# Performance work log

Measured on AMD Instinct MI355X. Metric: run time of the kernel, lower is better.

## Reference

```python
import jax, jax.numpy as jnp
import numpy as np

N, E, DIN, DH, DE, DOUT, G = 100000, 1600000, 64, 128, 16, 1, 256

def setup_inputs() -> dict:
    key = jax.random.key(0)
    ks = jax.random.split(key, 16)
    p = lambda k, s: (jax.random.normal(k, s, dtype=jnp.float32) * 0.05)
    return {
        "x": jax.random.normal(ks[0], (N, DIN), dtype=jnp.float32),
        "edge_index": jax.random.randint(ks[1], (2, E), 0, N, dtype=jnp.int64),
        "edge_attr": jax.random.normal(ks[2], (E, DE), dtype=jnp.float32),
        "batch": jnp.sort(jax.random.randint(ks[3], (N,), 0, G, dtype=jnp.int64)),
        # GINEConv 1: edge lin (edge_dim -> input_dim) + mlp1 (DIN->DH->DH)
        "ew1": p(ks[4], (DIN, DE)), "eb1": p(ks[5], (DIN,)),
        "w1a": p(ks[6], (DH, DIN)), "b1a": p(ks[7], (DH,)),
        "w1b": p(ks[8], (DH, DH)), "b1b": p(ks[9], (DH,)),
        # GINEConv 2: edge lin (edge_dim -> hidden_dim) + mlp2 (DH->DH->DH)
        "ew2": p(ks[10], (DH, DE)), "eb2": p(ks[11], (DH,)),
        "w2a": p(ks[12], (DH, DH)), "b2a": p(ks[13], (DH,)),
        "w2b": p(ks[14], (DH, DH)), "b2b": p(ks[15], (DH,)),
        "wf": p(jax.random.fold_in(key, 99), (DOUT, DH)),
        "bf": jnp.zeros((DOUT,), dtype=jnp.float32),
    }

def _gine(x, src, dst, edge_attr, ew, eb, wa, ba, wb, bb):
    # message = relu(x[src] + Lin(edge_attr)); sum-aggregate at dst; eps=0
    msg = jax.nn.relu(x[src] + edge_attr @ ew.T + eb)          # [E, D]
    aggr = jax.ops.segment_sum(msg, dst, num_segments=x.shape[0])
    h = x + aggr                                               # (1+eps)*x + aggr, eps=0
    h = jax.nn.relu(h @ wa.T + ba)
    return h @ wb.T + bb

def reference(x, edge_index, edge_attr, batch, ew1, eb1, w1a, b1a, w1b, b1b,
              ew2, eb2, w2a, b2a, w2b, b2b, wf, bf):
    src, dst = edge_index[0], edge_index[1]
    h = _gine(x, src, dst, edge_attr, ew1, eb1, w1a, b1a, w1b, b1b)
    h = jax.nn.relu(h)  # dropout is identity in eval mode
    h = _gine(h, src, dst, edge_attr, ew2, eb2, w2a, b2a, w2b, b2b)
    h = jax.nn.relu(h)
    # global mean pool over graphs
    sums = jax.ops.segment_sum(h, batch, num_segments=G)       # [G, DH]
    cnts = jax.ops.segment_sum(jnp.ones((h.shape[0],), h.dtype), batch, num_segments=G)
    pooled = sums / jnp.maximum(cnts, 1.0)[:, None]
    return pooled @ wf.T + bf                                  # [G, DOUT]
```

## Files before the change

### kernel.cpp

```cpp
#include <hip/hip_runtime.h>

#define DINc 64
#define DHc  128
#define DEc  16
#define Gc   256
#define Rrep 64
#define SCB  1024

typedef unsigned short u16;
typedef unsigned int   u32;
typedef __attribute__((ext_vector_type(8))) short bf8;
typedef __attribute__((ext_vector_type(4))) short bf4;
typedef __attribute__((ext_vector_type(4))) float f4;
typedef __attribute__((ext_vector_type(4))) unsigned int u32x4;
typedef _Float16 h2t __attribute__((ext_vector_type(2)));

__device__ __forceinline__ u16 f2b(float f) {
  u32 u = __builtin_bit_cast(u32, f);
  u32 r = u + 0x7FFFu + ((u >> 16) & 1u);
  return (u16)(r >> 16);
}
__device__ __forceinline__ float b2f(u16 h) {
  u32 u = ((u32)h) << 16;
  return __builtin_bit_cast(float, u);
}
__device__ __forceinline__ float blo(u32 v) {
  return __builtin_bit_cast(float, v << 16);
}
__device__ __forceinline__ float bhi(u32 v) {
  return __builtin_bit_cast(float, v & 0xFFFF0000u);
}
__device__ __forceinline__ u32 pkbf(float a, float b) {
  return ((u32)f2b(b) << 16) | (u32)f2b(a);
}
__device__ __forceinline__ u32 pkh(float a, float b) {
  u16 ua = __builtin_bit_cast(u16, (_Float16)a);
  u16 ub = __builtin_bit_cast(u16, (_Float16)b);
  return ((u32)ub << 16) | ua;
}
__device__ __forceinline__ float fd2(u32 a, u32 b, float c) {
  return __builtin_amdgcn_fdot2(__builtin_bit_cast(h2t, a),
                                __builtin_bit_cast(h2t, b), c, false);
}

__global__ __launch_bounds__(256) void k_cvtw(const float* __restrict__ w1a,
                                              const float* __restrict__ w1b,
                                              const float* __restrict__ w2a,
                                              const float* __restrict__ w2b,
                                              u16* __restrict__ dst) {
  const int i = blockIdx.x * 256 + threadIdx.x;
  const float* src; int off;
  if      (i < 1024) { src = w1a; off = i; }
  else if (i < 3072) { src = w1b; off = i - 1024; }
  else if (i < 5120) { src = w2a; off = i - 3072; }
  else if (i < 7168) { src = w2b; off = i - 5120; }
  else return;
  float4 f0 = *(const float4*)(src + (size_t)off * 8);
  float4 f1 = *(const float4*)(src + (size_t)off * 8 + 4);
  bf8 v;
  v[0]=(short)f2b(f0.x); v[1]=(short)f2b(f0.y); v[2]=(short)f2b(f0.z); v[3]=(short)f2b(f0.w);
  v[4]=(short)f2b(f1.x); v[5]=(short)f2b(f1.y); v[6]=(short)f2b(f1.z); v[7]=(short)f2b(f1.w);
  *(bf8*)(dst + (size_t)i * 8) = v;
}

__global__ __launch_bounds__(256) void k_hist(const int* __restrict__ dstA, const int nE,
                                              int* __restrict__ deg) {
  for (int i = blockIdx.x * 256 + threadIdx.x; i < nE; i += gridDim.x * 256)
    atomicAdd(&deg[dstA[i]], 1);
}

__global__ __launch_bounds__(256) void k_scan_blk(const int* __restrict__ deg,
                                                  int* __restrict__ bsum, const int nN) {
  const int b = blockIdx.x, t = threadIdx.x;
  const int i0 = b * SCB + t * 4;
  int s = 0;
  #pragma unroll
  for (int q = 0; q < 4; ++q) { const int i = i0 + q; if (i < nN) s += deg[i]; }
  #pragma unroll
  for (int off = 32; off > 0; off >>= 1) s += __shfl_down(s, off);
  __shared__ int ws[4];
  if ((t & 63) == 0) ws[t >> 6] = s;
  __syncthreads();
  if (t == 0) bsum[b] = ws[0] + ws[1] + ws[2] + ws[3];
}

__global__ __launch_bounds__(256) void k_scan_fin(const int* __restrict__ deg,
                                                  const int* __restrict__ bsum,
                                                  int* __restrict__ rowptr,
                                                  const int nN, const int nB) {
  const int b = blockIdx.x, t = threadIdx.x;
  int p = 0;
  for (int i = t; i < b; i += 256) p += bsum[i];
  #pragma unroll
  for (int off = 32; off > 0; off >>= 1) p += __shfl_down(p, off);
  __shared__ int ws[4];
  __shared__ int sc[256];
  if ((t & 63) == 0) ws[t >> 6] = p;
  const int i0 = b * SCB + t * 4;
  int vals[4]; int s = 0;
  #pragma unroll
  for (int q = 0; q < 4; ++q) { const int i = i0 + q; vals[q] = (i < nN) ? deg[i] : 0; s += vals[q]; }
  sc[t] = s;
  __syncthreads();
  const int boff = ws[0] + ws[1] + ws[2] + ws[3];
  for (int off = 1; off < 256; off <<= 1) {
    int u = (t >= off) ? sc[t - off] : 0;
    __syncthreads();
    sc[t] += u;
    __syncthreads();
  }
  int run = boff + sc[t] - s;
  #pragma unroll
  for (int q = 0; q < 4; ++q) { const int i = i0 + q; if (i < nN) rowptr[i] = run; run += vals[q]; }
  if (b == nB - 1 && t == 255) rowptr[nN] = run;
}

__global__ __launch_bounds__(256) void k_fill(const int* __restrict__ dstA,
                                              const int* __restrict__ srcA,
                                              const float* __restrict__ ea, const int nE,
                                              const int* __restrict__ rowptr,
                                              int* __restrict__ cursor,
                                              int* __restrict__ srcC,
                                              u16* __restrict__ ea16) {
  for (int i = blockIdx.x * 256 + threadIdx.x; i < nE; i += gridDim.x * 256) {
    const int d = dstA[i];
    const int pos = rowptr[d] + atomicAdd(&cursor[d], 1);
    srcC[pos] = srcA[i];
    const float4* ep = (const float4*)(ea + (size_t)i * 16);
    float4 a0 = ep[0], a1 = ep[1], a2 = ep[2], a3 = ep[3];
    u32x4 w0, w1;
    w0[0] = pkh(a0.x, a0.y); w0[1] = pkh(a0.z, a0.w);
    w0[2] = pkh(a1.x, a1.y); w0[3] = pkh(a1.z, a1.w);
    w1[0] = pkh(a2.x, a2.y); w1[1] = pkh(a2.z, a2.w);
    w1[2] = pkh(a3.x, a3.y); w1[3] = pkh(a3.z, a3.w);
    *(u32x4*)(ea16 + (size_t)pos * 16)     = w0;
    *(u32x4*)(ea16 + (size_t)pos * 16 + 8) = w1;
  }
}

__device__ __forceinline__ int span_lb(const int* __restrict__ rp, int nN, int target) {
  int lo = 0, hi = nN;
  while (lo < hi) { int m = (lo + hi) >> 1; if (rp[m] < target) lo = m + 1; else hi = m; }
  return lo;
}

template<int D, bool XF>
__global__ __launch_bounds__(256) void gather3(
    const float* __restrict__ xf, const u16* __restrict__ xb,
    const int* __restrict__ srcC, const u16* __restrict__ ea16,
    const float* __restrict__ ewg, const float* __restrict__ ebg,
    const int* __restrict__ rowptr, u16* __restrict__ agg,
    const int nN, const int nE)
{
  constexpr int PL = D / 64;
  __shared__ u32 eas[4][64][8];
  const int lane = threadIdx.x & 63, wv = threadIdx.x >> 6;
  u32 (*E)[8] = eas[wv];

  u32 wpk[8 * PL]; float ebr[PL];
  #pragma unroll
  for (int p = 0; p < PL; ++p) {
    const int d = lane * PL + p;
    ebr[p] = ebg[d];
    #pragma unroll
    for (int j = 0; j < 8; ++j)
      wpk[p * 8 + j] = pkh(ewg[d * 16 + 2 * j], ewg[d * 16 + 2 * j + 1]);
  }

  const int wgid = blockIdx.x * 4 + wv;
  const int nw   = gridDim.x * 4;
  const int t0 = (int)((long long)nE * wgid / nw);
  const int t1 = (int)((long long)nE * (wgid + 1) / nw);
  const int n0 = span_lb(rowptr, nN, t0);
  const int n1 = (wgid == nw - 1) ? nN : span_lb(rowptr, nN, t1);
  if (n0 >= n1) return;
  const int e1 = rowptr[n1];

  int nwb = n0;
  int rpv = rowptr[min(nwb + lane, n1)];
  int wbase = 0, wend = -1;
  int sidl = 0;

  for (int n = n0; n < n1; ++n) {
    int rel = n - nwb;
    if (rel >= 63) {
      nwb = n;
      rpv = rowptr[min(nwb + lane, n1)];
      rel = 0;
    }
    int p         = __builtin_amdgcn_readlane(rpv, rel);
    const int end = __builtin_amdgcn_readlane(rpv, rel + 1);
    float acc0 = 0.f, acc1 = 0.f;
    while (p < end) {
      if (p >= wend) {
        const int cw = min(64, e1 - p);
        if (lane < cw) {
          sidl = srcC[p + lane];
          u32x4 a = *(const u32x4*)(ea16 + (size_t)(p + lane) * 16);
          u32x4 b = *(const u32x4*)(ea16 + (size_t)(p + lane) * 16 + 8);
          *(u32x4*)&E[lane][0] = a;
          *(u32x4*)&E[lane][4] = b;
        }
        wbase = p; wend = p + cw;
      }
      const int k = min(end, wend) - p;
      for (int i = 0; i < k; i += 8) {
        const int g = min(8, k - i);
        u32 xv[8]; float xs[8];
        #pragma unroll
        for (int q = 0; q < 8; ++q) {
          if (q < g) {
            const int s = __builtin_amdgcn_readlane(sidl, p - wbase + i + q);
            if (XF) xs[q] = xf[(size_t)s * D + lane];
            else    xv[q] = *(const u32*)(xb + (size_t)s * D + lane * 2);
          }
        }
        #pragma unroll
        for (int q = 0; q < 8; ++q) {
          if (q < g) {
            const int e = p - wbase + i + q;
            u32x4 r0 = *(const u32x4*)&E[e][0];
            u32x4 r1 = *(const u32x4*)&E[e][4];
            if (PL == 1) {
              float v = ebr[0];
              v = fd2(r0[0], wpk[0], v); v = fd2(r0[1], wpk[1], v);
              v = fd2(r0[2], wpk[2], v); v = fd2(r0[3], wpk[3], v);
              v = fd2(r1[0], wpk[4], v); v = fd2(r1[1], wpk[5], v);
              v = fd2(r1[2], wpk[6], v); v = fd2(r1[3], wpk[7], v);
              const float xval = XF ? xs[q] : blo(xv[q]);
              acc0 += fmaxf(xval + v, 0.f);
            } else {
              float v0 = ebr[0], v1 = ebr[1];
              v0 = fd2(r0[0], wpk[0], v0); v1 = fd2(r0[0], wpk[8],  v1);
              v0 = fd2(r0[1], wpk[1], v0); v1 = fd2(r0[1], wpk[9],  v1);
              v0 = fd2(r0[2], wpk[2], v0); v1 = fd2(r0[2], wpk[10], v1);
              v0 = fd2(r0[3], wpk[3], v0); v1 = fd2(r0[3], wpk[11], v1);
              v0 = fd2(r1[0], wpk[4], v0); v1 = fd2(r1[0], wpk[12], v1);
              v0 = fd2(r1[1], wpk[5], v0); v1 = fd2(r1[1], wpk[13], v1);
              v0 = fd2(r1[2], wpk[6], v0); v1 = fd2(r1[2], wpk[14], v1);
              v0 = fd2(r1[3], wpk[7], v0); v1 = fd2(r1[3], wpk[15], v1);
              acc0 += fmaxf(blo(xv[q]) + v0, 0.f);
              acc1 += fmaxf(bhi(xv[q]) + v1, 0.f);
            }
          }
        }
      }
      p += k;
    }
    if (PL == 2) *(u32*)(agg + (size_t)n * 128 + lane * 2) = pkbf(acc0, acc1);
    else         agg[(size_t)n * 64 + lane] = f2b(acc0);
  }
}

template<int IN, bool XF>
__global__ __launch_bounds__(256) void k_l1(
    const float* __restrict__ xf, const u16* __restrict__ xbm,
    const u16* __restrict__ agb,
    const u16* __restrict__ waB, const float* __restrict__ ba,
    u16* __restrict__ tout, const int nN)
{
  __shared__ u16 wa_s[DHc * IN];
  __shared__ float ba_s[DHc];
  const int tid = threadIdx.x;
  constexpr int INC = IN / 8;
  for (int c = tid; c < DHc * INC; c += 256) {
    const int row = c / INC, kc = (c % INC) * 8;
    bf8 v = *(const bf8*)(waB + (size_t)row * IN + kc);
    *(bf8*)(wa_s + ((row * IN + kc) ^ ((row & 7) << 3))) = v;
  }
  if (tid < DHc) ba_s[tid] = ba[tid];
  __syncthreads();
  const int lane = tid & 63, wv = tid >> 6;
  const int lr = lane & 15, l4 = lane >> 4;
  const int nT = (nN + 15) >> 4;
  for (int tile = blockIdx.x * 4 + wv; tile < nT; tile += gridDim.x * 4) {
    const int node = tile * 16 + lr;
    const int n = min(node, nN - 1);
    bf8 bfr[IN / 32];
    #pragma unroll
    for (int ks = 0; ks < IN / 32; ++ks) {
      const int k0 = ks * 32 + l4 * 8;
      bf8 av = *(const bf8*)(agb + (size_t)n * IN + k0);
      bf8 v;
      if (XF) {
        float4 x0 = *(const float4*)(xf + (size_t)n * IN + k0);
        float4 x1 = *(const float4*)(xf + (size_t)n * IN + k0 + 4);
        v[0] = (short)f2b(x0.x + b2f((u16)av[0]));
        v[1] = (short)f2b(x0.y + b2f((u16)av[1]));
        v[2] = (short)f2b(x0.z + b2f((u16)av[2]));
        v[3] = (short)f2b(x0.w + b2f((u16)av[3]));
        v[4] = (short)f2b(x1.x + b2f((u16)av[4]));
        v[5] = (short)f2b(x1.y + b2f((u16)av[5]));
        v[6] = (short)f2b(x1.z + b2f((u16)av[6]));
        v[7] = (short)f2b(x1.w + b2f((u16)av[7]));
      } else {
        bf8 xv = *(const bf8*)(xbm + (size_t)n * IN + k0);
        #pragma unroll
        for (int j = 0; j < 8; ++j)
          v[j] = (short)f2b(b2f((u16)xv[j]) + b2f((u16)av[j]));
      }
      bfr[ks] = v;
    }
    const bool valid = node < nN;
    #pragma unroll
    for (int jt = 0; jt < 8; ++jt) {
      f4 c = {0.f, 0.f, 0.f, 0.f};
      #pragma unroll
      for (int ks = 0; ks < IN / 32; ++ks) {
        bf8 a = *(const bf8*)(wa_s + (((jt * 16 + lr) * IN + ks * 32 + l4 * 8) ^ ((lr & 7) << 3)));
        c = __builtin_amdgcn_mfma_f32_16x16x32_bf16(a, bfr[ks], c, 0, 0, 0);
      }
      if (valid) {
        float4 bav = *(const float4*)(ba_s + jt * 16 + l4 * 4);
        bf4 tv;
        tv[0] = (short)f2b(fmaxf(c[0] + bav.x, 0.f));
        tv[1] = (short)f2b(fmaxf(c[1] + bav.y, 0.f));
        tv[2] = (short)f2b(fmaxf(c[2] + bav.z, 0.f));
        tv[3] = (short)f2b(fmaxf(c[3] + bav.w, 0.f));
        *(bf4*)(tout + (size_t)node * DHc + jt * 16 + l4 * 4) = tv;
      }
    }
  }
}

template<bool FINAL>
__global__ __launch_bounds__(256) void k_l2(
    const u16* __restrict__ tin, const u16* __restrict__ wbB,
    const float* __restrict__ bb, u16* __restrict__ hout,
    const int* __restrict__ batch, float* __restrict__ sums, const int nN)
{
  __shared__ u16 wb_s[DHc * DHc];
  __shared__ float bb_s[DHc];
  const int tid = threadIdx.x;
  for (int c = tid; c < DHc * 16; c += 256) {
    const int row = c >> 4, kc = (c & 15) * 8;
    bf8 v = *(const bf8*)(wbB + (size_t)row * DHc + kc);
    *(bf8*)(wb_s + ((row * DHc + kc) ^ ((row & 7) << 3))) = v;
  }
  if (tid < DHc) bb_s[tid] = bb[tid];
  __syncthreads();
  const int lane = tid & 63, wv = tid >> 6;
  const int lr = lane & 15, l4 = lane >> 4;
  const int nT = (nN + 15) >> 4;
  const int gw0 = blockIdx.x * 4 + wv;
  const int rep = gw0 & (Rrep - 1);
  for (int tile = gw0; tile < nT; tile += gridDim.x * 4) {
    const int node0 = tile * 16;
    const int node = node0 + lr;
    const int n = min(node, nN - 1);
    bf8 tb[4];
    #pragma unroll
    for (int ks = 0; ks < 4; ++ks)
      tb[ks] = *(const bf8*)(tin + (size_t)n * DHc + ks * 32 + l4 * 8);
    const bool valid = node < nN;
    int gl = 0, g0 = 0; bool uni = false;
    if (FINAL) {
      gl = batch[n];
      g0 = __shfl(gl, 0);
      uni = __all(gl == g0) && (node0 + 16 <= nN);
    }
    #pragma unroll
    for (int jt = 0; jt < 8; ++jt) {
      f4 c = {0.f, 0.f, 0.f, 0.f};
      #pragma unroll
      for (int ks = 0; ks < 4; ++ks) {
        bf8 a = *(const bf8*)(wb_s + (((jt * 16 + lr) * DHc + ks * 32 + l4 * 8) ^ ((lr & 7) << 3)));
        c = __builtin_amdgcn_mfma_f32_16x16x32_bf16(a, tb[ks], c, 0, 0, 0);
      }
      float4 bbv = *(const float4*)(bb_s + jt * 16 + l4 * 4);
      float o0 = fmaxf(c[0] + bbv.x, 0.f);
      float o1 = fmaxf(c[1] + bbv.y, 0.f);
      float o2 = fmaxf(c[2] + bbv.z, 0.f);
      float o3 = fmaxf(c[3] + bbv.w, 0.f);
      if (!FINAL) {
        if (valid) {
          bf4 hv;
          hv[0] = (short)f2b(o0); hv[1] = (short)f2b(o1);
          hv[2] = (short)f2b(o2); hv[3] = (short)f2b(o3);
          *(bf4*)(hout + (size_t)node * DHc + jt * 16 + l4 * 4) = hv;
        }
      } else {
        if (uni) {
          #pragma unroll
          for (int off = 1; off < 16; off <<= 1) {
            o0 += __shfl_xor(o0, off);
            o1 += __shfl_xor(o1, off);
            o2 += __shfl_xor(o2, off);
            o3 += __shfl_xor(o3, off);
          }
          if (lr == 0) {
            float* dp = sums + ((size_t)rep * Gc + g0) * DHc + jt * 16 + l4 * 4;
            atomicAdd(dp + 0, o0); atomicAdd(dp + 1, o1);
            atomicAdd(dp + 2, o2); atomicAdd(dp + 3, o3);
          }
        } else if (valid) {
          float* dp = sums + ((size_t)rep * Gc + gl) * DHc + jt * 16 + l4 * 4;
          atomicAdd(dp + 0, o0); atomicAdd(dp + 1, o1);
          atomicAdd(dp + 2, o2); atomicAdd(dp + 3, o3);
        }
      }
    }
  }
}

__global__ __launch_bounds__(128) void pool_final(
    const float* __restrict__ sums, const int* __restrict__ batch,
    const float* __restrict__ wf, const float* __restrict__ bf,
    float* __restrict__ out, const int nN)
{
  const int g = blockIdx.x;
  const int j = threadIdx.x;
  float s = 0.f;
  for (int r = 0; r < Rrep; ++r) s += sums[((size_t)r * Gc + g) * DHc + j];
  int lo = 0, hi = nN;
  while (lo < hi) { int m = (lo + hi) >> 1; if (batch[m] < g) lo = m + 1; else hi = m; }
  int lo2 = lo, hi2 = nN;
  while (lo2 < hi2) { int m = (lo2 + hi2) >> 1; if (batch[m] < g + 1) lo2 = m + 1; else hi2 = m; }
  const float ct = fmaxf((float)(lo2 - lo), 1.f);
  __shared__ float red[128];
  red[j] = (s / ct) * wf[j];
  __syncthreads();
  for (int off = 64; off > 0; off >>= 1) { if (j < off) red[j] += red[j + off]; __syncthreads(); }
  if (j == 0) out[g] = red[0] + bf[0];
}

extern "C" void kernel_launch(void* const* d_in, const int* in_sizes, int n_in,
                              void* d_out, int out_size, void* d_ws, size_t ws_size,
                              hipStream_t stream) {
  const float* x    = (const float*)d_in[0];
  const int*   ei   = (const int*)d_in[1];
  const float* ea   = (const float*)d_in[2];
  const int*   batch= (const int*)d_in[3];
  const float* ew1  = (const float*)d_in[4];
  const float* eb1  = (const float*)d_in[5];
  const float* w1a  = (const float*)d_in[6];
  const float* b1a  = (const float*)d_in[7];
  const float* w1b  = (const float*)d_in[8];
  const float* b1b  = (const float*)d_in[9];
  const float* ew2  = (const float*)d_in[10];
  const float* eb2  = (const float*)d_in[11];
  const float* w2a  = (const float*)d_in[12];
  const float* b2a  = (const float*)d_in[13];
  const float* w2b  = (const float*)d_in[14];
  const float* b2b  = (const float*)d_in[15];
  const float* wf   = (const float*)d_in[16];
  const float* bf   = (const float*)d_in[17];
  float* out = (float*)d_out;

  const int nN = in_sizes[0] / DINc;
  const int nE = in_sizes[1] / 2;
  const int* srcA = ei;
  const int* dstA = ei + nE;

  char* wsb = (char*)d_ws;
  size_t o = 0;
  u16*   h1b    = (u16*)  (wsb + o); o += (size_t)nN * DHc * 2;
  u16*   tbuf   = (u16*)  (wsb + o); o += (size_t)nN * DHc * 2;
  u16*   agb    = (u16*)  (wsb + o); o += (size_t)nN * DHc * 2;
  float* sums   = (float*)(wsb + o); o += (size_t)Rrep * Gc * DHc * 4;
  int*   deg    = (int*)  (wsb + o); o += (size_t)nN * 4;
  int*   cursor = (int*)  (wsb + o); o += (size_t)nN * 4;
  int*   rowptr = (int*)  (wsb + o); o += (size_t)(nN + 1) * 4;
  int*   bsum   = (int*)  (wsb + o); o += (size_t)((nN + SCB - 1) / SCB) * 4; o = (o + 15) & ~(size_t)15;
  int*   srcC   = (int*)  (wsb + o); o += (size_t)nE * 4; o = (o + 15) & ~(size_t)15;
  u16*   ea16   = (u16*)  (wsb + o); o += (size_t)nE * 16 * 2;
  u16*   wts    = (u16*)  (wsb + o); o += (size_t)57344 * 2;
  u16* w1ab = wts;
  u16* w1bb = wts + 8192;
  u16* w2ab = wts + 8192 + 16384;
  u16* w2bb = wts + 8192 + 32768;
  (void)ws_size; (void)n_in; (void)out_size;

  hipMemsetAsync(sums, 0, (size_t)Rrep * Gc * DHc * 4, stream);
  hipMemsetAsync(deg, 0, (size_t)nN * 8, stream);

  const int nB = (nN + SCB - 1) / SCB;
  k_cvtw<<<28, 256, 0, stream>>>(w1a, w1b, w2a, w2b, wts);
  k_hist<<<1024, 256, 0, stream>>>(dstA, nE, deg);
  k_scan_blk<<<nB, 256, 0, stream>>>(deg, bsum, nN);
  k_scan_fin<<<nB, 256, 0, stream>>>(deg, bsum, rowptr, nN, nB);
  k_fill<<<1024, 256, 0, stream>>>(dstA, srcA, ea, nE, rowptr, cursor, srcC, ea16);

  const int nT = (nN + 15) / 16;
  const int mg = (nT + 3) / 4;
  gather3<DINc, true><<<2048, 256, 0, stream>>>(x, nullptr, srcC, ea16,
                                                ew1, eb1, rowptr, agb, nN, nE);
  k_l1<DINc, true><<<mg, 256, 0, stream>>>(x, nullptr, agb, w1ab, b1a, tbuf, nN);
  k_l2<false><<<mg, 256, 0, stream>>>(tbuf, w1bb, b1b, h1b, nullptr, nullptr, nN);
  gather3<DHc, false><<<2048, 256, 0, stream>>>(nullptr, h1b, srcC, ea16,
                                                ew2, eb2, rowptr, agb, nN, nE);
  k_l1<DHc, false><<<mg, 256, 0, stream>>>(nullptr, h1b, agb, w2ab, b2a, tbuf, nN);
  k_l2<true><<<mg, 256, 0, stream>>>(tbuf, w2bb, b2b, nullptr, batch, sums, nN);
  pool_final<<<Gc, 128, 0, stream>>>(sums, batch, wf, bf, out, nN);
}
```

Baseline: 642.5 us.

## Restructure gather into edge-chunk loop with ballot-detected node boundaries; merge prep kernels

The gather kernel now walks edges in fixed 64-edge chunks instead of node-by-node. It uses a new per-edge dst array (written in k_fill) and a ballot mask to find segment boundaries, so full chunks run a fast unrolled path with no per-node readlane or partial-chunk logic. The weight conversion and histogram kernels are merged into one launch. In exchange, k_fill writes an extra 6.4MB dstC array, the gather reads it back, and stores for empty nodes are emitted serially.

```diff
diff --git a/kernel.cpp b/kernel.cpp
--- a/kernel.cpp
+++ b/kernel.cpp
@@ -24,12 +24,8 @@
   u32 u = ((u32)h) << 16;
   return __builtin_bit_cast(float, u);
 }
-__device__ __forceinline__ float blo(u32 v) {
-  return __builtin_bit_cast(float, v << 16);
-}
-__device__ __forceinline__ float bhi(u32 v) {
-  return __builtin_bit_cast(float, v & 0xFFFF0000u);
-}
+__device__ __forceinline__ float blo(u32 v) { return __builtin_bit_cast(float, v << 16); }
+__device__ __forceinline__ float bhi(u32 v) { return __builtin_bit_cast(float, v & 0xFFFF0000u); }
 __device__ __forceinline__ u32 pkbf(float a, float b) {
   return ((u32)f2b(b) << 16) | (u32)f2b(a);
 }
@@ -43,30 +39,31 @@
                                 __builtin_bit_cast(h2t, b), c, false);
 }
 
-__global__ __launch_bounds__(256) void k_cvtw(const float* __restrict__ w1a,
-                                              const float* __restrict__ w1b,
-                                              const float* __restrict__ w2a,
-                                              const float* __restrict__ w2b,
-                                              u16* __restrict__ dst) {
-  const int i = blockIdx.x * 256 + threadIdx.x;
-  const float* src; int off;
-  if      (i < 1024) { src = w1a; off = i; }
-  else if (i < 3072) { src = w1b; off = i - 1024; }
-  else if (i < 5120) { src = w2a; off = i - 3072; }
-  else if (i < 7168) { src = w2b; off = i - 5120; }
-  else return;
-  float4 f0 = *(const float4*)(src + (size_t)off * 8);
-  float4 f1 = *(const float4*)(src + (size_t)off * 8 + 4);
-  bf8 v;
-  v[0]=(short)f2b(f0.x); v[1]=(short)f2b(f0.y); v[2]=(short)f2b(f0.z); v[3]=(short)f2b(f0.w);
-  v[4]=(short)f2b(f1.x); v[5]=(short)f2b(f1.y); v[6]=(short)f2b(f1.z); v[7]=(short)f2b(f1.w);
-  *(bf8*)(dst + (size_t)i * 8) = v;
-}
-
-__global__ __launch_bounds__(256) void k_hist(const int* __restrict__ dstA, const int nE,
-                                              int* __restrict__ deg) {
-  for (int i = blockIdx.x * 256 + threadIdx.x; i < nE; i += gridDim.x * 256)
-    atomicAdd(&deg[dstA[i]], 1);
+__global__ __launch_bounds__(256) void k_prep(
+    const float* __restrict__ w1a, const float* __restrict__ w1b,
+    const float* __restrict__ w2a, const float* __restrict__ w2b,
+    u16* __restrict__ wts,
+    const int* __restrict__ dstA, const int nE, int* __restrict__ deg) {
+  const int b = blockIdx.x;
+  if (b < 28) {
+    const int i = b * 256 + threadIdx.x;
+    const float* src; int off;
+    if      (i < 1024) { src = w1a; off = i; }
+    else if (i < 3072) { src = w1b; off = i - 1024; }
+    else if (i < 5120) { src = w2a; off = i - 3072; }
+    else if (i < 7168) { src = w2b; off = i - 5120; }
+    else return;
+    float4 f0 = *(const float4*)(src + (size_t)off * 8);
+    float4 f1 = *(const float4*)(src + (size_t)off * 8 + 4);
+    bf8 v;
+    v[0]=(short)f2b(f0.x); v[1]=(short)f2b(f0.y); v[2]=(short)f2b(f0.z); v[3]=(short)f2b(f0.w);
+    v[4]=(short)f2b(f1.x); v[5]=(short)f2b(f1.y); v[6]=(short)f2b(f1.z); v[7]=(short)f2b(f1.w);
+    *(bf8*)(wts + (size_t)i * 8) = v;
+  } else {
+    const int nb = gridDim.x - 28;
+    for (int i = (b - 28) * 256 + threadIdx.x; i < nE; i += nb * 256)
+      atomicAdd(&deg[dstA[i]], 1);
+  }
 }
 
 __global__ __launch_bounds__(256) void k_scan_blk(const int* __restrict__ deg,
@@ -121,11 +118,13 @@
                                               const int* __restrict__ rowptr,
                                               int* __restrict__ cursor,
                                               int* __restrict__ srcC,
+                                              int* __restrict__ dstC,
                                               u16* __restrict__ ea16) {
   for (int i = blockIdx.x * 256 + threadIdx.x; i < nE; i += gridDim.x * 256) {
     const int d = dstA[i];
     const int pos = rowptr[d] + atomicAdd(&cursor[d], 1);
     srcC[pos] = srcA[i];
+    dstC[pos] = d;
     const float4* ep = (const float4*)(ea + (size_t)i * 16);
     float4 a0 = ep[0], a1 = ep[1], a2 = ep[2], a3 = ep[3];
     u32x4 w0, w1;
@@ -144,10 +143,53 @@
   return lo;
 }
 
+#define STORE_N(NODE) do { \
+  if (PL == 2) *(u32*)(agg + (size_t)(NODE) * 128 + lane * 2) = pkbf(acc0, acc1); \
+  else         agg[(size_t)(NODE) * 64 + lane] = f2b(acc0); \
+} while (0)
+#define STORE_Z(NODE) do { \
+  if (PL == 2) *(u32*)(agg + (size_t)(NODE) * 128 + lane * 2) = 0u; \
+  else         agg[(size_t)(NODE) * 64 + lane] = 0; \
+} while (0)
+#define BCHK(EIDX) do { \
+  if ((bmask >> (EIDX)) & 1ull) { \
+    const int nd = __builtin_amdgcn_readlane(dl, (EIDX)); \
+    if (cur >= n0) STORE_N(cur); \
+    for (int m = cur + 1; m < nd; ++m) STORE_Z(m); \
+    acc0 = 0.f; acc1 = 0.f; cur = nd; \
+  } \
+} while (0)
+#define ACC_EDGE(EIDX, Q) do { \
+  u32x4 r0 = *(const u32x4*)&E[(EIDX)][0]; \
+  u32x4 r1 = *(const u32x4*)&E[(EIDX)][4]; \
+  if (PL == 1) { \
+    float v = ebr[0]; \
+    v = fd2(r0[0], wpk[0], v); v = fd2(r0[1], wpk[1], v); \
+    v = fd2(r0[2], wpk[2], v); v = fd2(r0[3], wpk[3], v); \
+    v = fd2(r1[0], wpk[4], v); v = fd2(r1[1], wpk[5], v); \
+    v = fd2(r1[2], wpk[6], v); v = fd2(r1[3], wpk[7], v); \
+    const float xval = XF ? xs[Q] : blo(xv[Q]); \
+    acc0 += fmaxf(xval + v, 0.f); \
+  } else { \
+    float v0 = ebr[0], v1 = ebr[1]; \
+    v0 = fd2(r0[0], wpk[0], v0); v1 = fd2(r0[0], wpk[8],  v1); \
+    v0 = fd2(r0[1], wpk[1], v0); v1 = fd2(r0[1], wpk[9],  v1); \
+    v0 = fd2(r0[2], wpk[2], v0); v1 = fd2(r0[2], wpk[10], v1); \
+    v0 = fd2(r0[3], wpk[3], v0); v1 = fd2(r0[3], wpk[11], v1); \
+    v0 = fd2(r1[0], wpk[4], v0); v1 = fd2(r1[0], wpk[12], v1); \
+    v0 = fd2(r1[1], wpk[5], v0); v1 = fd2(r1[1], wpk[13], v1); \
+    v0 = fd2(r1[2], wpk[6], v0); v1 = fd2(r1[2], wpk[14], v1); \
+    v0 = fd2(r1[3], wpk[7], v0); v1 = fd2(r1[3], wpk[15], v1); \
+    acc0 += fmaxf(blo(xv[Q]) + v0, 0.f); \
+    acc1 += fmaxf(bhi(xv[Q]) + v1, 0.f); \
+  } \
+} while (0)
+
 template<int D, bool XF>
-__global__ __launch_bounds__(256) void gather3(
+__global__ __launch_bounds__(256) void gather4(
     const float* __restrict__ xf, const u16* __restrict__ xb,
-    const int* __restrict__ srcC, const u16* __restrict__ ea16,
+    const int* __restrict__ srcC, const int* __restrict__ dstC,
+    const u16* __restrict__ ea16,
     const float* __restrict__ ewg, const float* __restrict__ ebg,
     const int* __restrict__ rowptr, u16* __restrict__ agg,
     const int nN, const int nE)
@@ -174,82 +216,66 @@
   const int n0 = span_lb(rowptr, nN, t0);
   const int n1 = (wgid == nw - 1) ? nN : span_lb(rowptr, nN, t1);
   if (n0 >= n1) return;
-  const int e1 = rowptr[n1];
-
-  int nwb = n0;
-  int rpv = rowptr[min(nwb + lane, n1)];
-  int wbase = 0, wend = -1;
-  int sidl = 0;
-
-  for (int n = n0; n < n1; ++n) {
-    int rel = n - nwb;
-    if (rel >= 63) {
-      nwb = n;
-      rpv = rowptr[min(nwb + lane, n1)];
-      rel = 0;
+  const int e0 = rowptr[n0], e1 = rowptr[n1];
+
+  float acc0 = 0.f, acc1 = 0.f;
+  int cur = n0 - 1;
+
+  for (int chunk = e0; chunk < e1; chunk += 64) {
+    const int cnt = min(64, e1 - chunk);
+    int sid = (lane < cnt) ? srcC[chunk + lane] : 0;
+    int dl  = (lane < cnt) ? dstC[chunk + lane] : -1;
+    const int pd = __shfl_up(dl, 1);
+    const bool bnd = (lane < cnt) && (dl != ((lane == 0) ? cur : pd));
+    const unsigned long long bmask = __ballot(bnd);
+
+    if (lane < cnt) {
+      u32x4 a = *(const u32x4*)(ea16 + (size_t)(chunk + lane) * 16);
+      u32x4 b = *(const u32x4*)(ea16 + (size_t)(chunk + lane) * 16 + 8);
+      *(u32x4*)&E[lane][0] = a;
+      *(u32x4*)&E[lane][4] = b;
     }
-    int p         = __builtin_amdgcn_readlane(rpv, rel);
-    const int end = __builtin_amdgcn_readlane(rpv, rel + 1);
-    float acc0 = 0.f, acc1 = 0.f;
-    while (p < end) {
-      if (p >= wend) {
-        const int cw = min(64, e1 - p);
-        if (lane < cw) {
-          sidl = srcC[p + lane];
-          u32x4 a = *(const u32x4*)(ea16 + (size_t)(p + lane) * 16);
-          u32x4 b = *(const u32x4*)(ea16 + (size_t)(p + lane) * 16 + 8);
-          *(u32x4*)&E[lane][0] = a;
-          *(u32x4*)&E[lane][4] = b;
+
+    if (cnt == 64) {
+      #pragma unroll 1
+      for (int i = 0; i < 64; i += 8) {
+        u32 xv[8]; float xs[8];
+        #pragma unroll
+        for (int q = 0; q < 8; ++q) {
+          const int s = __builtin_amdgcn_readlane(sid, i + q);
+          if (XF) xs[q] = xf[(size_t)s * D + lane];
+          else    xv[q] = *(const u32*)(xb + (size_t)s * D + lane * 2);
         }
-        wbase = p; wend = p + cw;
-      }
-      const int k = min(end, wend) - p;
-      for (int i = 0; i < k; i += 8) {
-        const int g = min(8, k - i);
+        const u32 gm = (u32)(bmask >> i) & 0xFFu;
+        if (gm == 0) {
+          #pragma unroll
+          for (int q = 0; q < 8; ++q) ACC_EDGE(i + q, q);
+        } else {
+          #pragma unroll
+          for (int q = 0; q < 8; ++q) { BCHK(i + q); ACC_EDGE(i + q, q); }
+        }
+      }
+    } else {
+      for (int i = 0; i < cnt; i += 8) {
+        const int g = min(8, cnt - i);
         u32 xv[8]; float xs[8];
         #pragma unroll
         for (int q = 0; q < 8; ++q) {
           if (q < g) {
-            const int s = __builtin_amdgcn_readlane(sidl, p - wbase + i + q);
+            const int s = __builtin_amdgcn_readlane(sid, i + q);
             if (XF) xs[q] = xf[(size_t)s * D + lane];
             else    xv[q] = *(const u32*)(xb + (size_t)s * D + lane * 2);
           }
         }
         #pragma unroll
         for (int q = 0; q < 8; ++q) {
-          if (q < g) {
-            const int e = p - wbase + i + q;
-            u32x4 r0 = *(const u32x4*)&E[e][0];
-            u32x4 r1 = *(const u32x4*)&E[e][4];
-            if (PL == 1) {
-              float v = ebr[0];
-              v = fd2(r0[0], wpk[0], v); v = fd2(r0[1], wpk[1], v);
-              v = fd2(r0[2], wpk[2], v); v = fd2(r0[3], wpk[3], v);
-              v = fd2(r1[0], wpk[4], v); v = fd2(r1[1], wpk[5], v);
-              v = fd2(r1[2], wpk[6], v); v = fd2(r1[3], wpk[7], v);
-              const float xval = XF ? xs[q] : blo(xv[q]);
-              acc0 += fmaxf(xval + v, 0.f);
-            } else {
-              float v0 = ebr[0], v1 = ebr[1];
-              v0 = fd2(r0[0], wpk[0], v0); v1 = fd2(r0[0], wpk[8],  v1);
-              v0 = fd2(r0[1], wpk[1], v0); v1 = fd2(r0[1], wpk[9],  v1);
-              v0 = fd2(r0[2], wpk[2], v0); v1 = fd2(r0[2], wpk[10], v1);
-              v0 = fd2(r0[3], wpk[3], v0); v1 = fd2(r0[3], wpk[11], v1);
-              v0 = fd2(r1[0], wpk[4], v0); v1 = fd2(r1[0], wpk[12], v1);
-              v0 = fd2(r1[1], wpk[5], v0); v1 = fd2(r1[1], wpk[13], v1);
-              v0 = fd2(r1[2], wpk[6], v0); v1 = fd2(r1[2], wpk[14], v1);
-              v0 = fd2(r1[3], wpk[7], v0); v1 = fd2(r1[3], wpk[15], v1);
-              acc0 += fmaxf(blo(xv[q]) + v0, 0.f);
-              acc1 += fmaxf(bhi(xv[q]) + v1, 0.f);
-            }
-          }
+          if (q < g) { BCHK(i + q); ACC_EDGE(i + q, q); }
         }
       }
-      p += k;
     }
-    if (PL == 2) *(u32*)(agg + (size_t)n * 128 + lane * 2) = pkbf(acc0, acc1);
-    else         agg[(size_t)n * 64 + lane] = f2b(acc0);
-  }
+  }
+  if (cur >= n0) STORE_N(cur);
+  for (int m = cur + 1; m < n1; ++m) STORE_Z(m);
 }
 
 template<int IN, bool XF>
@@ -462,7 +488,8 @@
   int*   cursor = (int*)  (wsb + o); o += (size_t)nN * 4;
   int*   rowptr = (int*)  (wsb + o); o += (size_t)(nN + 1) * 4;
   int*   bsum   = (int*)  (wsb + o); o += (size_t)((nN + SCB - 1) / SCB) * 4; o = (o + 15) & ~(size_t)15;
-  int*   srcC   = (int*)  (wsb + o); o += (size_t)nE * 4; o = (o + 15) & ~(size_t)15;
+  int*   srcC   = (int*)  (wsb + o); o += (size_t)nE * 4;
+  int*   dstC   = (int*)  (wsb + o); o += (size_t)nE * 4; o = (o + 15) & ~(size_t)15;
   u16*   ea16   = (u16*)  (wsb + o); o += (size_t)nE * 16 * 2;
   u16*   wts    = (u16*)  (wsb + o); o += (size_t)57344 * 2;
   u16* w1ab = wts;
@@ -475,19 +502,18 @@
   hipMemsetAsync(deg, 0, (size_t)nN * 8, stream);
 
   const int nB = (nN + SCB - 1) / SCB;
-  k_cvtw<<<28, 256, 0, stream>>>(w1a, w1b, w2a, w2b, wts);
-  k_hist<<<1024, 256, 0, stream>>>(dstA, nE, deg);
+  k_prep<<<28 + 512, 256, 0, stream>>>(w1a, w1b, w2a, w2b, wts, dstA, nE, deg);
   k_scan_blk<<<nB, 256, 0, stream>>>(deg, bsum, nN);
   k_scan_fin<<<nB, 256, 0, stream>>>(deg, bsum, rowptr, nN, nB);
-  k_fill<<<1024, 256, 0, stream>>>(dstA, srcA, ea, nE, rowptr, cursor, srcC, ea16);
+  k_fill<<<1024, 256, 0, stream>>>(dstA, srcA, ea, nE, rowptr, cursor, srcC, dstC, ea16);
 
   const int nT = (nN + 15) / 16;
   const int mg = (nT + 3) / 4;
-  gather3<DINc, true><<<2048, 256, 0, stream>>>(x, nullptr, srcC, ea16,
+  gather4<DINc, true><<<2048, 256, 0, stream>>>(x, nullptr, srcC, dstC, ea16,
                                                 ew1, eb1, rowptr, agb, nN, nE);
   k_l1<DINc, true><<<mg, 256, 0, stream>>>(x, nullptr, agb, w1ab, b1a, tbuf, nN);
   k_l2<false><<<mg, 256, 0, stream>>>(tbuf, w1bb, b1b, h1b, nullptr, nullptr, nN);
-  gather3<DHc, false><<<2048, 256, 0, stream>>>(nullptr, h1b, srcC, ea16,
+  gather4<DHc, false><<<2048, 256, 0, stream>>>(nullptr, h1b, srcC, dstC, ea16,
                                                 ew2, eb2, rowptr, agb, nN, nE);
   k_l1<DHc, false><<<mg, 256, 0, stream>>>(nullptr, h1b, agb, w2ab, b2a, tbuf, nN);
   k_l2<true><<<mg, 256, 0, stream>>>(tbuf, w2bb, b2b, nullptr, batch, sums, nN);
```

Result: faster. 574.8 us (-10.5%).
